# Performance work log

Measured on AMD Instinct MI355X. Metric: run time of the kernel, lower is better.

Reference implementation:

```python
import jax, jax.numpy as jnp
import numpy as np

GROUPS = 32
EPS = 1e-6


def group_norm(x, gamma, beta):
    b, h, w, c = x.shape
    xg = x.reshape(b, h, w, GROUPS, c // GROUPS)
    mean = jnp.mean(xg, axis=(1, 2, 4), keepdims=True)
    var = jnp.var(xg, axis=(1, 2, 4), keepdims=True)
    xn = ((xg - mean) * jax.lax.rsqrt(var + EPS)).reshape(b, h, w, c)
    return xn * gamma + beta


def conv1x1(x, w, b):
    # 1x1 conv == per-pixel matmul over channels
    return jnp.einsum('bhwc,cd->bhwd', x, w) + b


def setup_inputs() -> dict:
    key = jax.random.key(0)
    ks = jax.random.split(key, 10)
    b, h, w, c = 32, 32, 32, 512
    scale = 1.0 / np.sqrt(c)
    return {
        'x': jax.random.normal(ks[0], (b, h, w, c), dtype=jnp.float32),
        'gn_gamma': jnp.ones((c,), dtype=jnp.float32),
        'gn_beta': jnp.zeros((c,), dtype=jnp.float32),
        'wq': jax.random.normal(ks[1], (c, c), dtype=jnp.float32) * scale,
        'bq': jnp.zeros((c,), dtype=jnp.float32),
        'wk': jax.random.normal(ks[2], (c, c), dtype=jnp.float32) * scale,
        'bk': jnp.zeros((c,), dtype=jnp.float32),
        'wv': jax.random.normal(ks[3], (c, c), dtype=jnp.float32) * scale,
        'bv': jnp.zeros((c,), dtype=jnp.float32),
        'wo': jax.random.normal(ks[4], (c, c), dtype=jnp.float32) * scale,
        'bo': jnp.zeros((c,), dtype=jnp.float32),
    }


def reference(x, gn_gamma, gn_beta, wq, bq, wk, bk, wv, bv, wo, bo):
    previous = x
    xn = group_norm(x, gn_gamma, gn_beta)
    q = conv1x1(xn, wq, bq)
    k = conv1x1(xn, wk, bk)
    v = conv1x1(xn, wv, bv)
    b, h, w, c = q.shape
    hw = h * w
    # Faithful to original TF code: raw row-major reshape of channels-last
    # tensor to (b, c, h*w) WITHOUT transpose (reinterprets memory layout).
    q = q.reshape(b, c, hw)
    k = k.reshape(b, c, hw)
    v = v.reshape(b, c, hw)
    q = jnp.transpose(q, (0, 2, 1))              # (b, hw, c)
    s = (q @ k) * (c ** -0.5)                    # (b, hw, hw)
    s = jax.nn.softmax(s, axis=-1)
    s = jnp.transpose(s, (0, 2, 1))              # (b, hw, hw)
    out = v @ s                                  # (b, c, hw)
    out = out.reshape(b, h, w, c)                # raw reshape, matches TF
    return conv1x1(out, wo, bo) + previous
```

## Files before the change

### kernel.cpp

```cpp
#include <hip/hip_runtime.h>
#include <hip/hip_bf16.h>

#define B_   32
#define HW_  1024
#define C_   512
#define G_   32
#define CG_  16
#define NPIX (B_*HW_)

typedef short bf16x8 __attribute__((ext_vector_type(8)));
typedef float f32x4  __attribute__((ext_vector_type(4)));
using bf16 = __hip_bfloat16;

__device__ __forceinline__ void gload16(const void* g, void* l) {
    __builtin_amdgcn_global_load_lds((const __attribute__((address_space(1))) void*)g,
                                     (__attribute__((address_space(3))) void*)l, 16, 0, 0);
}

__global__ void wt_kernel(const float* __restrict__ w0, const float* __restrict__ w1,
                          const float* __restrict__ w2, const float* __restrict__ w3,
                          bf16* __restrict__ out) {
    __shared__ float tile[32][33];
    const float* src = blockIdx.z == 0 ? w0 : blockIdx.z == 1 ? w1 : blockIdx.z == 2 ? w2 : w3;
    bf16* dst = out + (size_t)blockIdx.z * C_ * C_;
    int r0 = blockIdx.y * 32, c0 = blockIdx.x * 32;
    int tx = threadIdx.x, ty = threadIdx.y;
    for (int i = 0; i < 32; i += 8)
        tile[ty + i][tx] = src[(size_t)(r0 + ty + i) * C_ + c0 + tx];
    __syncthreads();
    for (int i = 0; i < 32; i += 8)
        dst[(size_t)(c0 + ty + i) * C_ + r0 + tx] = __float2bfloat16(tile[tx][ty + i]);
}

__global__ void biascat_kernel(const float* __restrict__ bq, const float* __restrict__ bk,
                               const float* __restrict__ bv, float* __restrict__ o) {
    int i = blockIdx.x * 256 + threadIdx.x;
    const float* s = i < 512 ? bq : i < 1024 ? bk : bv;
    o[i] = s[i & 511];
}

__global__ void gn_stats_kernel(const float* __restrict__ x, float* __restrict__ mean,
                                float* __restrict__ rstd) {
    int b = blockIdx.x >> 5, g = blockIdx.x & 31;
    const float* xp = x + (size_t)b * HW_ * C_ + g * CG_;
    float s = 0.f, ss = 0.f;
    for (int p = threadIdx.x; p < HW_; p += 256) {
        const float4* v = (const float4*)(xp + (size_t)p * C_);
        #pragma unroll
        for (int j = 0; j < 4; ++j) {
            float4 t = v[j];
            s  += t.x + t.y + t.z + t.w;
            ss += t.x*t.x + t.y*t.y + t.z*t.z + t.w*t.w;
        }
    }
    #pragma unroll
    for (int off = 32; off; off >>= 1) { s += __shfl_down(s, off); ss += __shfl_down(ss, off); }
    __shared__ float red[2][4];
    int lane = threadIdx.x & 63, wv = threadIdx.x >> 6;
    if (lane == 0) { red[0][wv] = s; red[1][wv] = ss; }
    __syncthreads();
    if (threadIdx.x == 0) {
        float S  = red[0][0] + red[0][1] + red[0][2] + red[0][3];
        float SS = red[1][0] + red[1][1] + red[1][2] + red[1][3];
        const float inv_n = 1.f / (HW_ * CG_);
        float m = S * inv_n;
        float var = SS * inv_n - m * m;
        mean[blockIdx.x] = m;
        rstd[blockIdx.x] = rsqrtf(var + 1e-6f);
    }
}

__global__ void gn_apply_kernel(const float* __restrict__ x, const float* __restrict__ mean,
                                const float* __restrict__ rstd, const float* __restrict__ gamma,
                                const float* __restrict__ beta, bf16* __restrict__ xn) {
    const size_t n4 = (size_t)NPIX * C_ / 4;
    for (size_t i4 = (size_t)blockIdx.x * blockDim.x + threadIdx.x; i4 < n4;
         i4 += (size_t)gridDim.x * blockDim.x) {
        size_t e = i4 * 4;
        int cc = (int)(e & (C_ - 1));
        int bg = (int)(e >> 19) * G_ + (cc >> 4);
        float m = mean[bg], rs = rstd[bg];
        float4 t = *(const float4*)(x + e);
        __align__(8) bf16 o[4];
        o[0] = __float2bfloat16((t.x - m) * rs * gamma[cc + 0] + beta[cc + 0]);
        o[1] = __float2bfloat16((t.y - m) * rs * gamma[cc + 1] + beta[cc + 1]);
        o[2] = __float2bfloat16((t.z - m) * rs * gamma[cc + 2] + beta[cc + 2]);
        o[3] = __float2bfloat16((t.w - m) * rs * gamma[cc + 3] + beta[cc + 3]);
        *(ushort4*)(xn + e) = *(ushort4*)o;
    }
}

__global__ void transpose_kernel(const bf16* __restrict__ in, bf16* __restrict__ out,
                                 int R, int Cc) {
    __shared__ bf16 tile[64][65];
    size_t boff = (size_t)blockIdx.z * R * Cc;
    const bf16* src = in + boff;
    bf16* dst = out + boff;
    int c0 = blockIdx.x * 64, r0 = blockIdx.y * 64;
    int tx = threadIdx.x, ty = threadIdx.y;
    for (int i = 0; i < 64; i += 4)
        tile[ty + i][tx] = src[(size_t)(r0 + ty + i) * Cc + c0 + tx];
    __syncthreads();
    for (int i = 0; i < 64; i += 4)
        dst[(size_t)(c0 + ty + i) * R + r0 + tx] = tile[tx][ty + i];
}

template<int OUT_MODE>
__global__ __launch_bounds__(256) void gemm_kernel(
    const bf16* __restrict__ A, const bf16* __restrict__ Bt, void* __restrict__ Cv,
    const float* __restrict__ bias, const float* __restrict__ aux,
    int M, int N, int K, float scale,
    long long strideA, long long strideB, long long strideC)
{
    __shared__ __align__(16) ushort la[128 * 32];
    __shared__ __align__(16) ushort lb[128 * 32];

    int gx = gridDim.x, gy = gridDim.y;
    int nwg = gx * gy * (int)gridDim.z;
    int d = blockIdx.x + gx * (blockIdx.y + gy * blockIdx.z);
    int orig = (d & 7) * (nwg >> 3) + (d >> 3);
    int bx = orig % gx, rest = orig / gx;
    int by = rest % gy, bz = rest / gy;

    const bf16* Ab = A + (size_t)bz * strideA;
    const bf16* Bb = Bt + (size_t)bz * strideB;
    int m0 = by * 128, n0 = bx * 128;
    int t = threadIdx.x;
    int wv = t >> 6, lane = t & 63;
    int wm = wv >> 1, wn = wv & 1;
    int lrow = lane & 15, kg = lane >> 4;
    int slot8 = (kg ^ ((lrow >> 1) & 3)) << 3;

    int srow = lane >> 2;
    int gslot = (lane & 3) ^ ((srow >> 1) & 3);
    long long arow0 = (long long)(m0 + wv * 32 + srow) * K + gslot * 8;
    long long brow0 = (long long)(n0 + wv * 32 + srow) * K + gslot * 8;

    f32x4 acc[4][4] = {};

    for (int k0 = 0; k0 < K; k0 += 32) {
        #pragma unroll
        for (int cc = 0; cc < 2; ++cc) {
            gload16(Ab + arow0 + (long long)cc * 16 * K + k0, (char*)la + (wv * 2 + cc) * 1024);
            gload16(Bb + brow0 + (long long)cc * 16 * K + k0, (char*)lb + (wv * 2 + cc) * 1024);
        }
        __syncthreads();
        bf16x8 af[4], bg[4];
        #pragma unroll
        for (int f = 0; f < 4; ++f) {
            af[f] = *(const bf16x8*)&la[(wm * 64 + f * 16 + lrow) * 32 + slot8];
            bg[f] = *(const bf16x8*)&lb[(wn * 64 + f * 16 + lrow) * 32 + slot8];
        }
        #pragma unroll
        for (int i = 0; i < 4; ++i)
            #pragma unroll
            for (int j = 0; j < 4; ++j)
                acc[i][j] = __builtin_amdgcn_mfma_f32_16x16x32_bf16(af[i], bg[j], acc[i][j], 0, 0, 0);
        __syncthreads();
    }

    int rg = lane >> 4, ccol = lane & 15;

    if (OUT_MODE == 5) {
        float rowsum[16];
        #pragma unroll
        for (int u = 0; u < 16; ++u) rowsum[u] = 0.f;
        #pragma unroll
        for (int i = 0; i < 4; ++i)
            #pragma unroll
            for (int j = 0; j < 4; ++j) {
                int gcol = n0 + wn * 64 + j * 16 + ccol;
                int rowb = m0 + wm * 64 + i * 16 + rg * 4;
                #pragma unroll
                for (int r = 0; r < 4; ++r) {
                    float e = __expf(fminf(acc[i][j][r] * scale, 60.f));
                    rowsum[i * 4 + r] += e;
                    ((bf16*)Cv)[(size_t)bz * strideC + (size_t)(rowb + r) * N + gcol] =
                        __float2bfloat16(e);
                }
            }
        #pragma unroll
        for (int off = 1; off < 16; off <<= 1)
            #pragma unroll
            for (int u = 0; u < 16; ++u) rowsum[u] += __shfl_xor(rowsum[u], off);
        float* lsum = (float*)aux;
        #pragma unroll
        for (int u = 0; u < 16; ++u)
            if (ccol == u) {
                int row = m0 + wm * 64 + (u >> 2) * 16 + rg * 4 + (u & 3);
                atomicAdd(&lsum[(size_t)bz * 1024 + row], rowsum[u]);
            }
        return;
    }

    float linv[4];
    if (OUT_MODE == 6) {
        const float* lsum = aux;
        #pragma unroll
        for (int j = 0; j < 4; ++j)
            linv[j] = 1.f / lsum[(size_t)bz * 1024 + n0 + wn * 64 + j * 16 + ccol];
    }

    #pragma unroll
    for (int i = 0; i < 4; ++i)
        #pragma unroll
        for (int j = 0; j < 4; ++j) {
            int gcol = n0 + wn * 64 + j * 16 + ccol;
            int grow_base = m0 + wm * 64 + i * 16 + rg * 4;
            #pragma unroll
            for (int r = 0; r < 4; ++r) {
                float v = acc[i][j][r];
                if (OUT_MODE == 4) {
                    size_t idx = (size_t)(gcol >> 9) * ((size_t)NPIX * C_)
                               + (size_t)(grow_base + r) * C_ + (gcol & 511);
                    ((bf16*)Cv)[idx] = __float2bfloat16(v + bias[gcol]);
                } else {
                    size_t idx = (size_t)bz * strideC + (size_t)(grow_base + r) * N + gcol;
                    if (OUT_MODE == 6)      ((bf16*)Cv)[idx] = __float2bfloat16(v * linv[j]);
                    else                    ((float*)Cv)[idx] = v + bias[gcol] + ((const float*)aux)[idx];
                }
            }
        }
}

extern "C" void kernel_launch(void* const* d_in, const int* in_sizes, int n_in,
                              void* d_out, int out_size, void* d_ws, size_t ws_size,
                              hipStream_t stream) {
    const float* x     = (const float*)d_in[0];
    const float* gamma = (const float*)d_in[1];
    const float* beta  = (const float*)d_in[2];
    const float* wq    = (const float*)d_in[3];
    const float* bq    = (const float*)d_in[4];
    const float* wk    = (const float*)d_in[5];
    const float* bk    = (const float*)d_in[6];
    const float* wv    = (const float*)d_in[7];
    const float* bv    = (const float*)d_in[8];
    const float* wo    = (const float*)d_in[9];
    const float* bo    = (const float*)d_in[10];
    float* out = (float*)d_out;

    char* ws = (char*)d_ws;
    const size_t MB = 1ull << 20;
    bf16*  Wt   = (bf16*)ws;
    float* mean = (float*)(ws + 2 * MB);
    float* rstd = mean + 1024;
    float* bqkv = (float*)(ws + 2 * MB + 16384);
    float* lsum = (float*)(ws + 3 * MB);
    bf16*  xn   = (bf16*)(ws + 4 * MB);
    bf16*  q    = (bf16*)(ws + 36 * MB);
    bf16*  k    = (bf16*)(ws + 68 * MB);
    bf16*  v    = (bf16*)(ws + 100 * MB);
    bf16*  qt   = (bf16*)(ws + 132 * MB);
    bf16*  kt   = (bf16*)(ws + 164 * MB);
    bf16*  P    = (bf16*)(ws + 36 * MB);
    bf16*  outr = (bf16*)(ws + 132 * MB);

    const long long SB = 524288;
    const long long SS = 1048576;
    const float scale = 0.04419417382415922f;

    hipMemsetAsync(lsum, 0, 32 * 1024 * sizeof(float), stream);
    wt_kernel<<<dim3(16, 16, 4), dim3(32, 8), 0, stream>>>(wq, wk, wv, wo, Wt);
    biascat_kernel<<<6, 256, 0, stream>>>(bq, bk, bv, bqkv);
    gn_stats_kernel<<<1024, 256, 0, stream>>>(x, mean, rstd);
    gn_apply_kernel<<<4096, 256, 0, stream>>>(x, mean, rstd, gamma, beta, xn);

    gemm_kernel<4><<<dim3(12, 256, 1), 256, 0, stream>>>(
        xn, Wt, q, bqkv, nullptr, NPIX, 1536, C_, 1.f, 0, 0, 0);

    transpose_kernel<<<dim3(16, 8, 32), dim3(64, 4), 0, stream>>>(q, qt, 512, 1024);
    transpose_kernel<<<dim3(16, 8, 32), dim3(64, 4), 0, stream>>>(k, kt, 512, 1024);

    gemm_kernel<5><<<dim3(8, 8, 32), 256, 0, stream>>>(
        qt, kt, P, nullptr, lsum, 1024, 1024, 512, scale, SB, SB, SS);

    gemm_kernel<6><<<dim3(8, 4, 32), 256, 0, stream>>>(
        v, P, outr, nullptr, lsum, 512, 1024, 1024, 1.f, SB, SS, SB);

    gemm_kernel<3><<<dim3(4, 256, 1), 256, 0, stream>>>(
        outr, Wt + 3 * C_ * C_, out, bo, x, NPIX, C_, C_, 1.f, 0, 0, 0);
}
```

Before: 449.7 us.

## Rewrite GEMM as 256x256 tiled, 8-wave, double-buffered pipelined kernel

```diff
diff --git a/kernel.cpp b/kernel.cpp
--- a/kernel.cpp
+++ b/kernel.cpp
@@ -106,14 +106,14 @@
 }
 
 template<int OUT_MODE>
-__global__ __launch_bounds__(256) void gemm_kernel(
+__global__ __launch_bounds__(512, 2) void gemm_kernel(
     const bf16* __restrict__ A, const bf16* __restrict__ Bt, void* __restrict__ Cv,
     const float* __restrict__ bias, const float* __restrict__ aux,
     int M, int N, int K, float scale,
     long long strideA, long long strideB, long long strideC)
 {
-    __shared__ __align__(16) ushort la[128 * 32];
-    __shared__ __align__(16) ushort lb[128 * 32];
+    __shared__ __align__(16) ushort ldsA[2][2][8192];
+    __shared__ __align__(16) ushort ldsB[2][2][8192];
 
     int gx = gridDim.x, gy = gridDim.y;
     int nwg = gx * gy * (int)gridDim.z;
@@ -124,53 +124,131 @@
 
     const bf16* Ab = A + (size_t)bz * strideA;
     const bf16* Bb = Bt + (size_t)bz * strideB;
-    int m0 = by * 128, n0 = bx * 128;
+    int m0 = by * 256, n0 = bx * 256;
     int t = threadIdx.x;
-    int wv = t >> 6, lane = t & 63;
-    int wm = wv >> 1, wn = wv & 1;
+    int wv8 = t >> 6, lane = t & 63;
+    int wm = wv8 >> 2, wn = wv8 & 3;
     int lrow = lane & 15, kg = lane >> 4;
-    int slot8 = (kg ^ ((lrow >> 1) & 3)) << 3;
-
-    int srow = lane >> 2;
-    int gslot = (lane & 3) ^ ((srow >> 1) & 3);
-    long long arow0 = (long long)(m0 + wv * 32 + srow) * K + gslot * 8;
-    long long brow0 = (long long)(n0 + wv * 32 + srow) * K + gslot * 8;
-
-    f32x4 acc[4][4] = {};
-
-    for (int k0 = 0; k0 < K; k0 += 32) {
-        #pragma unroll
-        for (int cc = 0; cc < 2; ++cc) {
-            gload16(Ab + arow0 + (long long)cc * 16 * K + k0, (char*)la + (wv * 2 + cc) * 1024);
-            gload16(Bb + brow0 + (long long)cc * 16 * K + k0, (char*)lb + (wv * 2 + cc) * 1024);
+    int rsw = lrow & 7;
+
+    long long soff = (long long)(t >> 3) * K + (((t & 7) ^ ((t >> 3) & 7)) << 3);
+    long long aoff = (long long)m0 * K + soff;
+    long long boff = (long long)n0 * K + soff;
+    int ldsbyte = wv8 * 1024;
+
+    f32x4 acc[8][4] = {};
+    bf16x8 afq[4][2], bg0[2][2], bg1[2][2];
+
+    auto stA = [&](int buf, int half, int kt) {
+        const bf16* g = Ab + aoff + (long long)half * 128 * K + (long long)kt * 64;
+        char* l = (char*)&ldsA[buf][half][0] + ldsbyte;
+        gload16(g, l);
+        gload16(g + 64ll * K, l + 8192);
+    };
+    auto stB = [&](int buf, int half, int kt) {
+        const bf16* g = Bb + boff + (long long)half * 128 * K + (long long)kt * 64;
+        char* l = (char*)&ldsB[buf][half][0] + ldsbyte;
+        gload16(g, l);
+        gload16(g + 64ll * K, l + 8192);
+    };
+    auto ldA = [&](int buf, int f0) {
+        const char* base = (const char*)&ldsA[buf][wm][0];
+        #pragma unroll
+        for (int f = 0; f < 4; ++f) {
+            int row = (f0 + f) * 16 + lrow;
+            #pragma unroll
+            for (int ks = 0; ks < 2; ++ks)
+                afq[f][ks] = *(const bf16x8*)(base + row * 128 + (((ks * 4 + kg) ^ rsw) << 4));
         }
-        __syncthreads();
-        bf16x8 af[4], bg[4];
-        #pragma unroll
-        for (int f = 0; f < 4; ++f) {
-            af[f] = *(const bf16x8*)&la[(wm * 64 + f * 16 + lrow) * 32 + slot8];
-            bg[f] = *(const bf16x8*)&lb[(wn * 64 + f * 16 + lrow) * 32 + slot8];
+    };
+    auto ldB = [&](int buf, int c0, bf16x8 (&bg)[2][2]) {
+        const char* base = (const char*)&ldsB[buf][wn >> 1][0];
+        #pragma unroll
+        for (int c = 0; c < 2; ++c) {
+            int col = (wn & 1) * 64 + (c0 + c) * 16 + lrow;
+            #pragma unroll
+            for (int ks = 0; ks < 2; ++ks)
+                bg[c][ks] = *(const bf16x8*)(base + col * 128 + (((ks * 4 + kg) ^ rsw) << 4));
         }
-        #pragma unroll
-        for (int i = 0; i < 4; ++i)
-            #pragma unroll
-            for (int j = 0; j < 4; ++j)
-                acc[i][j] = __builtin_amdgcn_mfma_f32_16x16x32_bf16(af[i], bg[j], acc[i][j], 0, 0, 0);
-        __syncthreads();
+    };
+    auto mma = [&](int fb, int cb, bf16x8 (&bg)[2][2]) {
+        __builtin_amdgcn_s_setprio(1);
+        #pragma unroll
+        for (int f = 0; f < 4; ++f)
+            #pragma unroll
+            for (int c = 0; c < 2; ++c)
+                #pragma unroll
+                for (int ks = 0; ks < 2; ++ks)
+                    acc[fb + f][cb + c] = __builtin_amdgcn_mfma_f32_16x16x32_bf16(
+                        afq[f][ks], bg[c][ks], acc[fb + f][cb + c], 0, 0, 0);
+        __builtin_amdgcn_s_setprio(0);
+    };
+
+#define BAR()    __builtin_amdgcn_s_barrier()
+#define LGKM0()  do { asm volatile("s_waitcnt lgkmcnt(0)" ::: "memory"); \
+                      __builtin_amdgcn_sched_barrier(0); } while (0)
+#define VM(n)    asm volatile("s_waitcnt vmcnt(" #n ")" ::: "memory")
+
+    stB(0, 0, 0); stB(0, 1, 0); stA(0, 0, 0); stA(0, 1, 0);
+    stB(1, 0, 1); stB(1, 1, 1);
+
+    int nkt = K >> 6, iters = nkt >> 1;
+    for (int i = 0; i < iters; ++i) {
+        int t1 = 2 * i + 1, t2 = 2 * i + 2, t3 = 2 * i + 3;
+        bool more = (i + 1 < iters);
+        VM(4); BAR();
+        stA(1, 0, t1);
+        ldA(0, 0); ldB(0, 0, bg0);
+        LGKM0();
+        mma(0, 0, bg0);
+        BAR();
+        stA(1, 1, t1);
+        ldB(0, 2, bg1);
+        LGKM0();
+        mma(0, 2, bg1);
+        BAR();
+        if (more) stB(0, 0, t2);
+        ldA(0, 4);
+        LGKM0();
+        mma(4, 2, bg1);
+        BAR();
+        if (more) stB(0, 1, t2);
+        __builtin_amdgcn_sched_barrier(0);
+        mma(4, 0, bg0);
+        if (more) VM(4); else VM(0);
+        BAR();
+        if (more) stA(0, 0, t2);
+        ldA(1, 0); ldB(1, 0, bg0);
+        LGKM0();
+        mma(0, 0, bg0);
+        BAR();
+        if (more) stA(0, 1, t2);
+        ldB(1, 2, bg1);
+        LGKM0();
+        mma(0, 2, bg1);
+        BAR();
+        if (more) stB(1, 0, t3);
+        ldA(1, 4);
+        LGKM0();
+        mma(4, 2, bg1);
+        BAR();
+        if (more) stB(1, 1, t3);
+        __builtin_amdgcn_sched_barrier(0);
+        mma(4, 0, bg0);
     }
 
     int rg = lane >> 4, ccol = lane & 15;
 
     if (OUT_MODE == 5) {
-        float rowsum[16];
-        #pragma unroll
-        for (int u = 0; u < 16; ++u) rowsum[u] = 0.f;
-        #pragma unroll
-        for (int i = 0; i < 4; ++i)
+        float rowsum[32];
+        #pragma unroll
+        for (int u = 0; u < 32; ++u) rowsum[u] = 0.f;
+        #pragma unroll
+        for (int i = 0; i < 8; ++i)
             #pragma unroll
             for (int j = 0; j < 4; ++j) {
                 int gcol = n0 + wn * 64 + j * 16 + ccol;
-                int rowb = m0 + wm * 64 + i * 16 + rg * 4;
+                int rowb = m0 + wm * 128 + i * 16 + rg * 4;
                 #pragma unroll
                 for (int r = 0; r < 4; ++r) {
                     float e = __expf(fminf(acc[i][j][r] * scale, 60.f));
@@ -182,12 +260,12 @@
         #pragma unroll
         for (int off = 1; off < 16; off <<= 1)
             #pragma unroll
-            for (int u = 0; u < 16; ++u) rowsum[u] += __shfl_xor(rowsum[u], off);
+            for (int u = 0; u < 32; ++u) rowsum[u] += __shfl_xor(rowsum[u], off);
         float* lsum = (float*)aux;
         #pragma unroll
-        for (int u = 0; u < 16; ++u)
-            if (ccol == u) {
-                int row = m0 + wm * 64 + (u >> 2) * 16 + rg * 4 + (u & 3);
+        for (int u = 0; u < 32; ++u)
+            if (ccol == (u & 15)) {
+                int row = m0 + wm * 128 + (u >> 2) * 16 + rg * 4 + (u & 3);
                 atomicAdd(&lsum[(size_t)bz * 1024 + row], rowsum[u]);
             }
         return;
@@ -202,11 +280,11 @@
     }
 
     #pragma unroll
-    for (int i = 0; i < 4; ++i)
+    for (int i = 0; i < 8; ++i)
         #pragma unroll
         for (int j = 0; j < 4; ++j) {
             int gcol = n0 + wn * 64 + j * 16 + ccol;
-            int grow_base = m0 + wm * 64 + i * 16 + rg * 4;
+            int grow_base = m0 + wm * 128 + i * 16 + rg * 4;
             #pragma unroll
             for (int r = 0; r < 4; ++r) {
                 float v = acc[i][j][r];
@@ -221,6 +299,9 @@
                 }
             }
         }
+#undef BAR
+#undef LGKM0
+#undef VM
 }
 
 extern "C" void kernel_launch(void* const* d_in, const int* in_sizes, int n_in,
@@ -265,18 +346,18 @@
     gn_stats_kernel<<<1024, 256, 0, stream>>>(x, mean, rstd);
     gn_apply_kernel<<<4096, 256, 0, stream>>>(x, mean, rstd, gamma, beta, xn);
 
-    gemm_kernel<4><<<dim3(12, 256, 1), 256, 0, stream>>>(
+    gemm_kernel<4><<<dim3(6, 128, 1), 512, 0, stream>>>(
         xn, Wt, q, bqkv, nullptr, NPIX, 1536, C_, 1.f, 0, 0, 0);
 
     transpose_kernel<<<dim3(16, 8, 32), dim3(64, 4), 0, stream>>>(q, qt, 512, 1024);
     transpose_kernel<<<dim3(16, 8, 32), dim3(64, 4), 0, stream>>>(k, kt, 512, 1024);
 
-    gemm_kernel<5><<<dim3(8, 8, 32), 256, 0, stream>>>(
+    gemm_kernel<5><<<dim3(4, 4, 32), 512, 0, stream>>>(
         qt, kt, P, nullptr, lsum, 1024, 1024, 512, scale, SB, SB, SS);
 
-    gemm_kernel<6><<<dim3(8, 4, 32), 256, 0, stream>>>(
+    gemm_kernel<6><<<dim3(4, 2, 32), 512, 0, stream>>>(
         v, P, outr, nullptr, lsum, 512, 1024, 1024, 1.f, SB, SS, SB);
 
-    gemm_kernel<3><<<dim3(4, 256, 1), 256, 0, stream>>>(
+    gemm_kernel<3><<<dim3(2, 128, 1), 512, 0, stream>>>(
         outr, Wt + 3 * C_ * C_, out, bo, x, NPIX, C_, C_, 1.f, 0, 0, 0);
 }
```

Result: faster. 395.8 us (-12.0%).
